# Optimization experiments

Hardware: AMD Instinct MI355X
Metric: run time of the kernel (lower is better)

## Reference

```python
import jax, jax.numpy as jnp
import numpy as np

N_NODES = 65536
N_EDGES = 1048576
HID = 128
NUM_FEAT = 128
NUM_LAYERS = 3
NUM_EXPERTS = 4
NUM_GRAPHS = 512
NUM_CLASSES = 10
TEMP = 0.1


def _hard_concrete(logits, key, temp=TEMP):
    u = jax.random.uniform(key, logits.shape, dtype=logits.dtype, minval=1e-6, maxval=1.0 - 1e-6)
    g = -jnp.log(-jnp.log(u + 1e-20) + 1e-20)
    y_soft = jax.nn.sigmoid((logits + g) / temp)
    y_hard = (y_soft > 0.5).astype(y_soft.dtype)
    # straight-through: forward hard, backward soft
    return y_hard + (y_soft - jax.lax.stop_gradient(y_soft))


def _gin_encoder(h, src, dst, w1, b1, w2, b2, eps, edge_weight=None):
    # GIN with optional scalar edge weights: agg = sum_{j->i} w_ij * h_j
    L = w1.shape[0]
    for l in range(L):
        msg = h[src]
        if edge_weight is not None:
            msg = msg * edge_weight[:, None]
        agg = jax.ops.segment_sum(msg, dst, num_segments=N_NODES)
        z = (1.0 + eps[l]) * h + agg
        z = jax.nn.relu(z @ w1[l] + b1[l]) @ w2[l] + b2[l]
        h = jax.nn.relu(z) if l < L - 1 else z
    return h


def _mean_pool(h, batch):
    s = jax.ops.segment_sum(h, batch, num_segments=NUM_GRAPHS)
    cnt = jax.ops.segment_sum(jnp.ones((h.shape[0], 1), h.dtype), batch, num_segments=NUM_GRAPHS)
    return s / jnp.maximum(cnt, 1.0)


def setup_inputs() -> dict:
    key = jax.random.key(0)
    ks = jax.random.split(key, 32)
    s = 0.05
    d = {}
    d['x'] = jax.random.normal(ks[0], (N_NODES, NUM_FEAT), dtype=jnp.float32)
    d['edge_index'] = jax.random.randint(ks[1], (2, N_EDGES), 0, N_NODES, dtype=jnp.int32)
    d['batch'] = jnp.sort(jax.random.randint(ks[2], (N_NODES,), 0, NUM_GRAPHS, dtype=jnp.int32))
    # causal encoder (layers stacked; F == HID so shapes are uniform)
    d['cw1'] = jax.random.normal(ks[3], (NUM_LAYERS, HID, HID), dtype=jnp.float32) * s
    d['cb1'] = jnp.zeros((NUM_LAYERS, HID), jnp.float32)
    d['cw2'] = jax.random.normal(ks[4], (NUM_LAYERS, HID, HID), dtype=jnp.float32) * s
    d['cb2'] = jnp.zeros((NUM_LAYERS, HID), jnp.float32)
    d['ceps'] = jnp.zeros((NUM_LAYERS,), jnp.float32)
    # classifier encoder
    d['kw1'] = jax.random.normal(ks[5], (NUM_LAYERS, HID, HID), dtype=jnp.float32) * s
    d['kb1'] = jnp.zeros((NUM_LAYERS, HID), jnp.float32)
    d['kw2'] = jax.random.normal(ks[6], (NUM_LAYERS, HID, HID), dtype=jnp.float32) * s
    d['kb2'] = jnp.zeros((NUM_LAYERS, HID), jnp.float32)
    d['keps'] = jnp.zeros((NUM_LAYERS,), jnp.float32)
    # per-expert node mask MLPs: HID -> HID -> 1
    d['nm_w1'] = jax.random.normal(ks[7], (NUM_EXPERTS, HID, HID), dtype=jnp.float32) * s
    d['nm_b1'] = jnp.zeros((NUM_EXPERTS, HID), jnp.float32)
    d['nm_w2'] = jax.random.normal(ks[8], (NUM_EXPERTS, HID, 1), dtype=jnp.float32) * s
    d['nm_b2'] = jnp.zeros((NUM_EXPERTS, 1), jnp.float32)
    # per-expert edge mask MLPs: 2*HID -> HID -> 1
    d['em_w1'] = jax.random.normal(ks[9], (NUM_EXPERTS, 2 * HID, HID), dtype=jnp.float32) * s
    d['em_b1'] = jnp.zeros((NUM_EXPERTS, HID), jnp.float32)
    d['em_w2'] = jax.random.normal(ks[10], (NUM_EXPERTS, HID, 1), dtype=jnp.float32) * s
    d['em_b2'] = jnp.zeros((NUM_EXPERTS, 1), jnp.float32)
    # per-expert feat mask MLPs: HID -> HID -> NUM_FEAT
    d['fm_w1'] = jax.random.normal(ks[11], (NUM_EXPERTS, HID, HID), dtype=jnp.float32) * s
    d['fm_b1'] = jnp.zeros((NUM_EXPERTS, HID), jnp.float32)
    d['fm_w2'] = jax.random.normal(ks[12], (NUM_EXPERTS, HID, NUM_FEAT), dtype=jnp.float32) * s
    d['fm_b2'] = jnp.zeros((NUM_EXPERTS, NUM_FEAT), jnp.float32)
    # per-expert classifiers
    d['cls_w'] = jax.random.normal(ks[13], (NUM_EXPERTS, HID, NUM_CLASSES), dtype=jnp.float32) * s
    d['cls_b'] = jnp.zeros((NUM_EXPERTS, NUM_CLASSES), jnp.float32)
    return d


def reference(x, edge_index, batch, cw1, cb1, cw2, cb2, ceps, kw1, kb1, kw2, kb2, keps,
              nm_w1, nm_b1, nm_w2, nm_b2, em_w1, em_b1, em_w2, em_b2,
              fm_w1, fm_b1, fm_w2, fm_b2, cls_w, cls_b):
    src, dst = edge_index[0], edge_index[1]
    Z = _gin_encoder(x, src, dst, cw1, cb1, cw2, cb2, ceps)  # [N, HID]
    edge_feat = jnp.concatenate([Z[src], Z[dst]], axis=1)     # [E, 2*HID]
    base_key = jax.random.key(42)
    node_masks, edge_masks, feat_masks = [], [], []
    h_stable_list, expert_logits = [], []
    for k in range(NUM_EXPERTS):
        kk = jax.random.split(jax.random.fold_in(base_key, k), 3)
        nl = jax.nn.relu(Z @ nm_w1[k] + nm_b1[k]) @ nm_w2[k] + nm_b2[k]          # [N,1]
        el = jax.nn.relu(edge_feat @ em_w1[k] + em_b1[k]) @ em_w2[k] + em_b2[k]  # [E,1]
        fl = jax.nn.relu(Z @ fm_w1[k] + fm_b1[k]) @ fm_w2[k] + fm_b2[k]          # [N,F]
        node_mask = _hard_concrete(nl, kk[0])
        edge_mask = _hard_concrete(el, kk[1])
        feat_mask = _hard_concrete(fl, kk[2])
        node_masks.append(node_mask)
        edge_masks.append(edge_mask)
        feat_masks.append(feat_mask)
        masked_x = x * node_mask * feat_mask
        ew = edge_mask[:, 0]
        masked_Z = _gin_encoder(masked_x, src, dst, kw1, kb1, kw2, kb2, keps, edge_weight=ew)
        h_st = _mean_pool(masked_Z, batch)                                        # [G, HID]
        h_stable_list.append(h_st)
        expert_logits.append(h_st @ cls_w[k] + cls_b[k])
    node_masks = jnp.stack(node_masks, axis=1)       # [N, K, 1]
    edge_masks = jnp.stack(edge_masks, axis=1)       # [E, K, 1]
    feat_masks = jnp.stack(feat_masks, axis=1)       # [N, K, F]
    h_stable = jnp.stack(h_stable_list, axis=1)      # [G, K, HID]
    expert_logits = jnp.stack(expert_logits, axis=1) # [G, K, C]
    h_orig = _mean_pool(Z, batch)                    # [G, HID]
    return expert_logits, h_stable, h_orig, node_masks, edge_masks, feat_masks
```

## Files before the change

### kernel.cpp

```cpp
#include <hip/hip_runtime.h>
#include <stdint.h>

#define N_NODESC 65536
#define N_EDGESC 1048576
#define HIDC 128
#define NUM_GRAPHSC 512
#define NUM_CLASSESC 10
#define NUM_EXPERTSC 4
#define NUM_LAYERSC 3

static const size_t NH = (size_t)N_NODESC * HIDC;

typedef __attribute__((ext_vector_type(8))) short short8v;
typedef __attribute__((ext_vector_type(4))) float float4v;

__host__ __device__ __forceinline__ uint32_t rotl32(uint32_t v, int r) {
  return (v << r) | (v >> (32 - r));
}
__host__ __device__ inline void threefry2x32(uint32_t k0, uint32_t k1,
                                             uint32_t x0, uint32_t x1,
                                             uint32_t* o0, uint32_t* o1) {
  uint32_t k2 = k0 ^ k1 ^ 0x1BD11BDAu;
  x0 += k0; x1 += k1;
#define TF_R(r) x0 += x1; x1 = rotl32(x1, r); x1 ^= x0;
  TF_R(13) TF_R(15) TF_R(26) TF_R(6)
  x0 += k1; x1 += k2 + 1u;
  TF_R(17) TF_R(29) TF_R(16) TF_R(24)
  x0 += k2; x1 += k0 + 2u;
  TF_R(13) TF_R(15) TF_R(26) TF_R(6)
  x0 += k0; x1 += k1 + 3u;
  TF_R(17) TF_R(29) TF_R(16) TF_R(24)
  x0 += k1; x1 += k2 + 4u;
  TF_R(13) TF_R(15) TF_R(26) TF_R(6)
  x0 += k2; x1 += k0 + 5u;
#undef TF_R
  *o0 = x0; *o1 = x1;
}

__device__ __forceinline__ float uniform_from_bits(uint32_t b) {
  float f = __uint_as_float((b >> 9) | 0x3f800000u) - 1.0f;
  const float mn = 1e-6f;
  const float mx = 1.0f - 1e-6f;
  return fmaxf(mn, __fadd_rn(__fmul_rn(f, __fsub_rn(mx, mn)), mn));
}

__device__ __forceinline__ float hc_decide(float l, uint32_t key0, uint32_t key1,
                                           uint32_t i) {
  uint32_t o0, o1;
  threefry2x32(key0, key1, 0u, i, &o0, &o1);
  float u = uniform_from_bits(o0 ^ o1);
  float tf = -__logf(u);
  float gf = -__logf(tf);
  float margf = l + gf;
  if (fabsf(margf) > 1e-4f) return (margf > 0.0f) ? 1.0f : 0.0f;
  float t32 = (float)(-log((double)u));
  float g32 = (float)(-log((double)t32));
  float m32 = __fadd_rn(l, g32);
  float q = m32 / 0.1f;
  float e32 = (float)exp(-(double)q);
  float den = __fadd_rn(1.0f, e32);
  float s = 1.0f / den;
  return (s > 0.5f) ? 1.0f : 0.0f;
}

__device__ __forceinline__ float bf2f(unsigned short u) {
  return __uint_as_float(((uint32_t)u) << 16);
}
__device__ __forceinline__ unsigned short f2bf(float v) {
  uint32_t u = __float_as_uint(v);
  return (unsigned short)((u + 0x7FFFu + ((u >> 16) & 1u)) >> 16);
}

__global__ void khist(const int* __restrict__ dst, int* __restrict__ deg) {
  int e = blockIdx.x * 256 + threadIdx.x;
  if (e < N_EDGESC) atomicAdd(&deg[dst[e]], 1);
}

__global__ void kscan(const int* __restrict__ deg, int* __restrict__ offs) {
  __shared__ int part[1024];
  int t = threadIdx.x;
  int base = t * 64;
  int s = 0;
  for (int i = 0; i < 64; ++i) s += deg[base + i];
  part[t] = s;
  __syncthreads();
  for (int off = 1; off < 1024; off <<= 1) {
    int v = 0;
    if (t >= off) v = part[t - off];
    __syncthreads();
    part[t] += v;
    __syncthreads();
  }
  int run = part[t] - s;
  for (int i = 0; i < 64; ++i) {
    int d = deg[base + i];
    offs[base + i] = run;
    run += d;
  }
  if (t == 1023) offs[N_NODESC] = run;
}

__global__ void kfill(const int* __restrict__ src, const int* __restrict__ dst,
                      int* __restrict__ curs, int* __restrict__ csr_src,
                      int* __restrict__ csr_eid) {
  int e = blockIdx.x * 256 + threadIdx.x;
  if (e >= N_EDGESC) return;
  int d = dst[e];
  int p = atomicAdd(&curs[d], 1);
  csr_src[p] = src[e];
  csr_eid[p] = e;
}

__global__ void ksort(const int* __restrict__ offs, int* __restrict__ csr_src,
                      int* __restrict__ csr_eid) {
  int n = blockIdx.x * 256 + threadIdx.x;
  if (n >= N_NODESC) return;
  int s = offs[n], e = offs[n + 1];
  for (int i = s + 1; i < e; ++i) {
    int ke = csr_eid[i], ks = csr_src[i];
    int j = i - 1;
    while (j >= s && csr_eid[j] > ke) {
      csr_eid[j + 1] = csr_eid[j];
      csr_src[j + 1] = csr_src[j];
      --j;
    }
    csr_eid[j + 1] = ke;
    csr_src[j + 1] = ks;
  }
}

__global__ void kbounds(const int* __restrict__ batch, int* __restrict__ bounds) {
  int g = threadIdx.x;
  int lo = 0, hi = N_NODESC;
  while (lo < hi) {
    int mid = (lo + hi) >> 1;
    if (batch[mid] < g) lo = mid + 1; else hi = mid;
  }
  bounds[g] = lo;
  if (g == 0) bounds[NUM_GRAPHSC] = N_NODESC;
}

__global__ void gather_z(const float* __restrict__ hin,
                         const int* __restrict__ offs,
                         const int* __restrict__ csr_src,
                         const float* __restrict__ epsArr, int l,
                         float* __restrict__ zout) {
  int gt = blockIdx.x * blockDim.x + threadIdx.x;
  int n = gt >> 6;
  int lane = gt & 63;
  if (n >= N_NODESC) return;
  int s = offs[n], e = offs[n + 1];
  float ax = 0.f, ay = 0.f;
  int i = s;
  for (; i + 4 <= e; i += 4) {
    int s0 = csr_src[i], s1 = csr_src[i + 1], s2 = csr_src[i + 2], s3 = csr_src[i + 3];
    const float2 v0 = *(const float2*)&hin[(size_t)s0 * HIDC + lane * 2];
    const float2 v1 = *(const float2*)&hin[(size_t)s1 * HIDC + lane * 2];
    const float2 v2 = *(const float2*)&hin[(size_t)s2 * HIDC + lane * 2];
    const float2 v3 = *(const float2*)&hin[(size_t)s3 * HIDC + lane * 2];
    ax = __fadd_rn(ax, v0.x); ay = __fadd_rn(ay, v0.y);
    ax = __fadd_rn(ax, v1.x); ay = __fadd_rn(ay, v1.y);
    ax = __fadd_rn(ax, v2.x); ay = __fadd_rn(ay, v2.y);
    ax = __fadd_rn(ax, v3.x); ay = __fadd_rn(ay, v3.y);
  }
  for (; i < e; ++i) {
    int sn = csr_src[i];
    const float2 v = *(const float2*)&hin[(size_t)sn * HIDC + lane * 2];
    ax = __fadd_rn(ax, v.x);
    ay = __fadd_rn(ay, v.y);
  }
  float ep = __fadd_rn(1.0f, epsArr[l]);
  const float2 hv = *(const float2*)&hin[(size_t)n * HIDC + lane * 2];
  ax = __fadd_rn(__fmul_rn(ep, hv.x), ax);
  ay = __fadd_rn(__fmul_rn(ep, hv.y), ay);
  float2 o; o.x = ax; o.y = ay;
  *(float2*)&zout[(size_t)n * HIDC + lane * 2] = o;
}

__device__ __forceinline__ int MXOR(int m) { return (m * 4) ^ ((m & 96) >> 1); }

__device__ __forceinline__ void gemm_body(const float* __restrict__ Xf,
                                          const float* __restrict__ W,
                                          const float* __restrict__ bias,
                                          float* __restrict__ Of,
                                          int doRelu, int tile) {
  __shared__ char sXb[64 * 512];
  __shared__ char sWb[64 * 512];
  const int tid = threadIdx.x;
  const size_t base = (size_t)tile * HIDC * HIDC;
  const int tm = (tid >> 4) << 3;
  const int tn = (tid & 15) << 3;
  const int xA = MXOR(tm), xA2 = MXOR(tm + 4);
  const int xB = MXOR(tn), xB2 = MXOR(tn + 4);

  float acc[8][8];
#pragma unroll
  for (int i = 0; i < 8; ++i)
#pragma unroll
    for (int j = 0; j < 8; ++j) acc[i][j] = 0.0f;

  for (int kh = 0; kh < 2; ++kh) {
    __syncthreads();
#pragma unroll
    for (int i = 0; i < 8; ++i) {
      int idx = tid + 256 * i;
      int m = idx >> 4;
      int kq = (idx & 15) * 4;
      float4 v = *(const float4*)(Xf + base + (size_t)m * HIDC + kh * 64 + kq);
      int mo = MXOR(m);
      *(float*)(sXb + (kq + 0) * 512 + mo) = v.x;
      *(float*)(sXb + (kq + 1) * 512 + mo) = v.y;
      *(float*)(sXb + (kq + 2) * 512 + mo) = v.z;
      *(float*)(sXb + (kq + 3) * 512 + mo) = v.w;
    }
#pragma unroll
    for (int i = 0; i < 8; ++i) {
      int idx = tid + 256 * i;
      int kk = idx >> 5;
      int n0 = (idx & 31) * 4;
      float4 v = *(const float4*)(W + (size_t)(kh * 64 + kk) * HIDC + n0);
      *(float4*)(sWb + kk * 512 + MXOR(n0)) = v;
    }
    __syncthreads();

#pragma unroll 4
    for (int kk = 0; kk < 64; ++kk) {
      float4 a0 = *(const float4*)(sXb + kk * 512 + xA);
      float4 a1 = *(const float4*)(sXb + kk * 512 + xA2);
      float4 b0 = *(const float4*)(sWb + kk * 512 + xB);
      float4 b1 = *(const float4*)(sWb + kk * 512 + xB2);
      float a[8] = {a0.x, a0.y, a0.z, a0.w, a1.x, a1.y, a1.z, a1.w};
      float b[8] = {b0.x, b0.y, b0.z, b0.w, b1.x, b1.y, b1.z, b1.w};
#pragma unroll
      for (int i = 0; i < 8; ++i)
#pragma unroll
        for (int j = 0; j < 8; ++j) acc[i][j] = fmaf(a[i], b[j], acc[i][j]);
    }
  }

  float bvals[8];
#pragma unroll
  for (int j = 0; j < 8; ++j) bvals[j] = bias ? bias[tn + j] : 0.0f;
#pragma unroll
  for (int i = 0; i < 8; ++i) {
    float r[8];
#pragma unroll
    for (int j = 0; j < 8; ++j) {
      float v = __fadd_rn(acc[i][j], bvals[j]);
      if (doRelu) v = fmaxf(v, 0.0f);
      r[j] = v;
    }
    size_t off = base + (size_t)(tm + i) * HIDC + tn;
    *(float4*)&Of[off] = *(float4*)&r[0];
    *(float4*)&Of[off + 4] = *(float4*)&r[4];
  }
}

__global__ __launch_bounds__(256, 2)
void gemm_f32(const float* __restrict__ X, const float* __restrict__ W,
              const float* __restrict__ bias, float* __restrict__ O, int doRelu) {
  gemm_body(X, W, bias, O, doRelu, blockIdx.x);
}

__global__ __launch_bounds__(256, 2)
void gemm_f32x4(const float* __restrict__ X,
                const float* W0, const float* W1, const float* W2, const float* W3,
                const float* b0, const float* b1,
                float* o0, float* o1, float* o2, float* o3) {
  int slice = blockIdx.x >> 9;
  int tile = blockIdx.x & 511;
  const float* W; const float* bias; float* O; int relu;
  if (slice == 0)      { W = W0; bias = b0; O = o0; relu = 1; }
  else if (slice == 1) { W = W1; bias = b1; O = o1; relu = 1; }
  else if (slice == 2) { W = W2; bias = nullptr; O = o2; relu = 0; }
  else                 { W = W3; bias = nullptr; O = o3; relu = 0; }
  gemm_body(X, W, bias, O, relu, tile);
}

__global__ void kprepW(const float* __restrict__ kw1, const float* __restrict__ kw2,
                       unsigned short* __restrict__ Wt) {
  int t = blockIdx.x * 256 + threadIdx.x;
  int mat = t >> 11;
  int r = t & 2047;
  int n = r >> 4;
  int kkc = r & 15;
  const float* W = (mat < 3) ? (kw1 + (size_t)mat * HIDC * HIDC)
                             : (kw2 + (size_t)(mat - 3) * HIDC * HIDC);
  unsigned short pk[8];
#pragma unroll
  for (int j = 0; j < 8; ++j)
    pk[j] = f2bf(W[(size_t)(kkc * 8 + j) * HIDC + n]);
  *(uint4*)(Wt + (size_t)mat * HIDC * HIDC + (size_t)n * HIDC + kkc * 8) =
      *(uint4*)pk;
}

__global__ __launch_bounds__(256, 2)
void gemm_mfma(const unsigned short* __restrict__ Xpool,
               const unsigned short* __restrict__ Wt,
               const float* __restrict__ bias,
               unsigned short* __restrict__ Opool, int doRelu) {
  __shared__ unsigned short sX[128 * 128];
  __shared__ unsigned short sW[128 * 128];
  const int tid = threadIdx.x;
  const int kex = blockIdx.x >> 9;
  const int tile = blockIdx.x & 511;
  const unsigned short* X = Xpool + (size_t)kex * NH + (size_t)tile * HIDC * HIDC;
  unsigned short* O = Opool + (size_t)kex * NH + (size_t)tile * HIDC * HIDC;

#pragma unroll
  for (int i = 0; i < 8; ++i) {
    int idx = tid + 256 * i;
    int r = idx >> 4;
    int cc = idx & 15;
    uint4 vx = *(const uint4*)(X + (size_t)r * HIDC + cc * 8);
    uint4 vw = *(const uint4*)(Wt + (size_t)r * HIDC + cc * 8);
    int sc = (cc ^ (r & 7)) * 8;
    *(uint4*)(sX + r * HIDC + sc) = vx;
    *(uint4*)(sW + r * HIDC + sc) = vw;
  }
  __syncthreads();

  const int lane = tid & 63;
  const int wid = tid >> 6;
  const int wm = wid * 32;
  const int lrow = lane & 15;
  const int lk = (lane >> 4) * 4;

  float4v acc[2][8];
#pragma unroll
  for (int rt = 0; rt < 2; ++rt)
#pragma unroll
    for (int nt = 0; nt < 8; ++nt) acc[rt][nt] = (float4v)0.0f;

  union FU { uint2 u2[2]; short8v s8; };

  for (int kc = 0; kc < 128; kc += 32) {
    int kb = kc + lk;
    int c0 = ((kb >> 3) ^ 0) * 8 + (kb & 7);
    short8v afr[2], bfr[8];
#pragma unroll
    for (int rt = 0; rt < 2; ++rt) {
      int row = wm + rt * 16 + lrow;
      const unsigned short* basep = sX + row * HIDC;
      int s0 = (((kb) >> 3) ^ (row & 7)) * 8 + (kb & 7);
      int s1 = (((kb + 16) >> 3) ^ (row & 7)) * 8 + (kb & 7);
      FU u;
      u.u2[0] = *(const uint2*)(basep + s0);
      u.u2[1] = *(const uint2*)(basep + s1);
      afr[rt] = u.s8;
    }
#pragma unroll
    for (int nt = 0; nt < 8; ++nt) {
      int row = nt * 16 + lrow;
      const unsigned short* basep = sW + row * HIDC;
      int s0 = (((kb) >> 3) ^ (row & 7)) * 8 + (kb & 7);
      int s1 = (((kb + 16) >> 3) ^ (row & 7)) * 8 + (kb & 7);
      FU u;
      u.u2[0] = *(const uint2*)(basep + s0);
      u.u2[1] = *(const uint2*)(basep + s1);
      bfr[nt] = u.s8;
    }
#pragma unroll
    for (int rt = 0; rt < 2; ++rt)
#pragma unroll
      for (int nt = 0; nt < 8; ++nt)
        acc[rt][nt] = __builtin_amdgcn_mfma_f32_16x16x32_bf16(
            afr[rt], bfr[nt], acc[rt][nt], 0, 0, 0);
    (void)c0;
  }

#pragma unroll
  for (int nt = 0; nt < 8; ++nt) {
    float bv = bias[nt * 16 + lrow];
#pragma unroll
    for (int rt = 0; rt < 2; ++rt) {
#pragma unroll
      for (int j = 0; j < 4; ++j) {
        float v = acc[rt][nt][j] + bv;
        if (doRelu) v = fmaxf(v, 0.0f);
        int row = wm + rt * 16 + (lane >> 4) * 4 + j;
        O[(size_t)row * HIDC + nt * 16 + lrow] = f2bf(v);
      }
    }
  }
}

__global__ void rowdot(const float* __restrict__ X, const float* __restrict__ w,
                       const float* __restrict__ bptr, uint32_t key0, uint32_t key1,
                       float* __restrict__ outp) {
  int gt = blockIdx.x * blockDim.x + threadIdx.x;
  int row = gt >> 6, lane = gt & 63;
  if (row >= N_NODESC) return;
  const float2 x = *(const float2*)&X[(size_t)row * HIDC + lane * 2];
  const float2 ww = *(const float2*)&w[lane * 2];
  float p = x.x * ww.x + x.y * ww.y;
#pragma unroll
  for (int m = 32; m; m >>= 1) p += __shfl_xor(p, m, 64);
  if (lane == 0) {
    float l = p + bptr[0];
    outp[(size_t)row * NUM_EXPERTSC] = hc_decide(l, key0, key1, (uint32_t)row);
  }
}

__global__ void edge_csrK(const float* __restrict__ A, const float* __restrict__ Bm,
                          const float* __restrict__ b1, const float* __restrict__ w2,
                          const float* __restrict__ b2,
                          const int* __restrict__ offs, const int* __restrict__ csr_src,
                          const int* __restrict__ csr_eid,
                          uint32_t key0, uint32_t key1,
                          float* __restrict__ outp, unsigned char* __restrict__ mcsr) {
  int n = blockIdx.x * 4 + (threadIdx.x >> 6);
  int lane = threadIdx.x & 63;
  int g = lane >> 4;
  int gl = lane & 15;
  const float4* Bv = (const float4*)&Bm[(size_t)n * HIDC + gl * 8];
  float4 b_lo = Bv[0], b_hi = Bv[1];
  float4 bb_lo = *(const float4*)&b1[gl * 8];
  float4 bb_hi = *(const float4*)&b1[gl * 8 + 4];
  float4 w_lo = *(const float4*)&w2[gl * 8];
  float4 w_hi = *(const float4*)&w2[gl * 8 + 4];
  float bscalar = b2[0];
  int s = offs[n], e = offs[n + 1];
  for (int i = s; i < e; i += 4) {
    int cnt = e - i; if (cnt > 4) cnt = 4;
    float p = 0.0f;
    if (g < cnt) {
      int sg = csr_src[i + g];
      const float4* Av = (const float4*)&A[(size_t)sg * HIDC + gl * 8];
      float4 a_lo = Av[0], a_hi = Av[1];
      float h;
      h = fmaxf(__fadd_rn(__fadd_rn(a_lo.x, b_lo.x), bb_lo.x), 0.0f); p = fmaf(h, w_lo.x, p);
      h = fmaxf(__fadd_rn(__fadd_rn(a_lo.y, b_lo.y), bb_lo.y), 0.0f); p = fmaf(h, w_lo.y, p);
      h = fmaxf(__fadd_rn(__fadd_rn(a_lo.z, b_lo.z), bb_lo.z), 0.0f); p = fmaf(h, w_lo.z, p);
      h = fmaxf(__fadd_rn(__fadd_rn(a_lo.w, b_lo.w), bb_lo.w), 0.0f); p = fmaf(h, w_lo.w, p);
      h = fmaxf(__fadd_rn(__fadd_rn(a_hi.x, b_hi.x), bb_hi.x), 0.0f); p = fmaf(h, w_hi.x, p);
      h = fmaxf(__fadd_rn(__fadd_rn(a_hi.y, b_hi.y), bb_hi.y), 0.0f); p = fmaf(h, w_hi.y, p);
      h = fmaxf(__fadd_rn(__fadd_rn(a_hi.z, b_hi.z), bb_hi.z), 0.0f); p = fmaf(h, w_hi.z, p);
      h = fmaxf(__fadd_rn(__fadd_rn(a_hi.w, b_hi.w), bb_hi.w), 0.0f); p = fmaf(h, w_hi.w, p);
    }
    p += __shfl_xor(p, 1, 16);
    p += __shfl_xor(p, 2, 16);
    p += __shfl_xor(p, 4, 16);
    p += __shfl_xor(p, 8, 16);
    if (g < cnt && gl == 0) {
      int eid = csr_eid[i + g];
      float l = p + bscalar;
      float mval = hc_decide(l, key0, key1, (uint32_t)eid);
      outp[(size_t)eid * NUM_EXPERTSC] = mval;
      mcsr[i + g] = (unsigned char)mval;
    }
  }
}

__global__ void ksampleF(const float* __restrict__ lg, uint32_t key0, uint32_t key1,
                         float* __restrict__ outp) {
  int i = blockIdx.x * 256 + threadIdx.x;
  float m = hc_decide(lg[i], key0, key1, (uint32_t)i);
  outp[(size_t)(i >> 7) * (NUM_EXPERTSC * HIDC) + (i & 127)] = m;
}

__global__ void kmaskxB(const float* __restrict__ x, const float* __restrict__ nmaskb,
                        const float* __restrict__ fmaskb,
                        unsigned short* __restrict__ hbpool) {
  int k = blockIdx.x >> 13;
  int t = (blockIdx.x & 8191) * 256 + threadIdx.x;
  int n = t >> 5;
  int q = (t & 31) << 2;
  float nm = nmaskb[(size_t)n * NUM_EXPERTSC + k];
  float4 xv = *(const float4*)&x[(size_t)n * HIDC + q];
  float4 fv = *(const float4*)&fmaskb[(size_t)n * (NUM_EXPERTSC * HIDC) + k * HIDC + q];
  ushort2 p0, p1;
  p0.x = f2bf(xv.x * nm * fv.x); p0.y = f2bf(xv.y * nm * fv.y);
  p1.x = f2bf(xv.z * nm * fv.z); p1.y = f2bf(xv.w * nm * fv.w);
  uint2 pk; pk.x = (uint32_t)p0.x | ((uint32_t)p0.y << 16);
  pk.y = (uint32_t)p1.x | ((uint32_t)p1.y << 16);
  *(uint2*)(hbpool + (size_t)k * NH + (size_t)n * HIDC + q) = pk;
}

__global__ void gatherC(const unsigned short* __restrict__ hpool,
                        const int* __restrict__ offs,
                        const int* __restrict__ csr_src,
                        const unsigned char* __restrict__ mcsr,
                        const float* __restrict__ epsArr, int l,
                        unsigned short* __restrict__ aggpool) {
  int gid = blockIdx.x * 4 + (threadIdx.x >> 6);
  int lane = threadIdx.x & 63;
  int k = gid >> 16;
  int n = gid & 65535;
  const unsigned short* h = hpool + (size_t)k * NH;
  const unsigned char* mc = mcsr + (size_t)k * N_EDGESC;
  int s = offs[n], e = offs[n + 1];
  float ax = 0.f, ay = 0.f;
  for (int base = s; base < e; base += 64) {
    int j = base + lane;
    int valid = (j < e);
    int keep = valid ? (mc[j] != 0) : 0;
    int srcj = valid ? csr_src[j] : 0;
    unsigned long long ball = __ballot(keep);
    while (ball) {
      int l0 = -1, l1 = -1, l2 = -1, l3 = -1;
      l0 = __ffsll((unsigned long long)ball) - 1; ball &= ball - 1;
      if (ball) { l1 = __ffsll((unsigned long long)ball) - 1; ball &= ball - 1; }
      if (ball) { l2 = __ffsll((unsigned long long)ball) - 1; ball &= ball - 1; }
      if (ball) { l3 = __ffsll((unsigned long long)ball) - 1; ball &= ball - 1; }
      int s0 = __shfl(srcj, l0, 64);
      int s1 = (l1 >= 0) ? __shfl(srcj, l1, 64) : 0;
      int s2 = (l2 >= 0) ? __shfl(srcj, l2, 64) : 0;
      int s3 = (l3 >= 0) ? __shfl(srcj, l3, 64) : 0;
      uint32_t v0 = *(const uint32_t*)(h + (size_t)s0 * HIDC + lane * 2);
      uint32_t v1 = (l1 >= 0) ? *(const uint32_t*)(h + (size_t)s1 * HIDC + lane * 2) : 0;
      uint32_t v2 = (l2 >= 0) ? *(const uint32_t*)(h + (size_t)s2 * HIDC + lane * 2) : 0;
      uint32_t v3 = (l3 >= 0) ? *(const uint32_t*)(h + (size_t)s3 * HIDC + lane * 2) : 0;
      ax += __uint_as_float(v0 << 16); ay += __uint_as_float(v0 & 0xFFFF0000u);
      if (l1 >= 0) { ax += __uint_as_float(v1 << 16); ay += __uint_as_float(v1 & 0xFFFF0000u); }
      if (l2 >= 0) { ax += __uint_as_float(v2 << 16); ay += __uint_as_float(v2 & 0xFFFF0000u); }
      if (l3 >= 0) { ax += __uint_as_float(v3 << 16); ay += __uint_as_float(v3 & 0xFFFF0000u); }
    }
  }
  float ep = 1.0f + epsArr[l];
  uint32_t hv = *(const uint32_t*)(h + (size_t)n * HIDC + lane * 2);
  ax = fmaf(ep, __uint_as_float(hv << 16), ax);
  ay = fmaf(ep, __uint_as_float(hv & 0xFFFF0000u), ay);
  uint32_t pk = (uint32_t)f2bf(ax) | ((uint32_t)f2bf(ay) << 16);
  *(uint32_t*)(aggpool + (size_t)k * NH + (size_t)n * HIDC + lane * 2) = pk;
}

__global__ void pool(const float* __restrict__ h, const int* __restrict__ bounds,
                     float* __restrict__ outp, int rowStride) {
  int g = blockIdx.x, j = threadIdx.x;
  int s = bounds[g], e = bounds[g + 1];
  float acc = 0.0f;
  for (int i = s; i < e; ++i) acc = __fadd_rn(acc, h[(size_t)i * HIDC + j]);
  int cnt = e - s; if (cnt < 1) cnt = 1;
  outp[(size_t)g * rowStride + j] = acc / (float)cnt;
}

__global__ void poolB(const unsigned short* __restrict__ hbpool,
                      const int* __restrict__ bounds, float* __restrict__ outp) {
  int k = blockIdx.x >> 9;
  int g = blockIdx.x & 511;
  int j = threadIdx.x;
  const unsigned short* h = hbpool + (size_t)k * NH;
  int s = bounds[g], e = bounds[g + 1];
  float acc = 0.0f;
  for (int i = s; i < e; ++i) acc += bf2f(h[(size_t)i * HIDC + j]);
  int cnt = e - s; if (cnt < 1) cnt = 1;
  outp[(size_t)g * (NUM_EXPERTSC * HIDC) + k * HIDC + j] = acc / (float)cnt;
}

__global__ void kclsB(const float* __restrict__ hst, const float* __restrict__ w,
                      const float* __restrict__ b, float* __restrict__ outp) {
  int k = blockIdx.x >> 9;
  int g = blockIdx.x & 511;
  int c = threadIdx.x;
  if (c >= NUM_CLASSESC) return;
  float acc = 0.0f;
  for (int j = 0; j < HIDC; ++j)
    acc = __fadd_rn(acc, __fmul_rn(hst[(size_t)g * (NUM_EXPERTSC * HIDC) + k * HIDC + j],
                                   w[(size_t)k * HIDC * NUM_CLASSESC + j * NUM_CLASSESC + c]));
  outp[(size_t)g * (NUM_EXPERTSC * NUM_CLASSESC) + k * NUM_CLASSESC + c] =
      acc + b[k * NUM_CLASSESC + c];
}

extern "C" void kernel_launch(void* const* d_in, const int* in_sizes, int n_in,
                              void* d_out, int out_size, void* d_ws, size_t ws_size,
                              hipStream_t stream) {
  const float* x    = (const float*)d_in[0];
  const int* eidx   = (const int*)d_in[1];
  const int* batch  = (const int*)d_in[2];
  const float* cw1  = (const float*)d_in[3];
  const float* cb1  = (const float*)d_in[4];
  const float* cw2  = (const float*)d_in[5];
  const float* cb2  = (const float*)d_in[6];
  const float* ceps = (const float*)d_in[7];
  const float* kw1  = (const float*)d_in[8];
  const float* kb1  = (const float*)d_in[9];
  const float* kw2  = (const float*)d_in[10];
  const float* kb2  = (const float*)d_in[11];
  const float* keps = (const float*)d_in[12];
  const float* nm_w1 = (const float*)d_in[13];
  const float* nm_b1 = (const float*)d_in[14];
  const float* nm_w2 = (const float*)d_in[15];
  const float* nm_b2 = (const float*)d_in[16];
  const float* em_w1 = (const float*)d_in[17];
  const float* em_b1 = (const float*)d_in[18];
  const float* em_w2 = (const float*)d_in[19];
  const float* em_b2 = (const float*)d_in[20];
  const float* fm_w1 = (const float*)d_in[21];
  const float* fm_b1 = (const float*)d_in[22];
  const float* fm_w2 = (const float*)d_in[23];
  const float* fm_b2 = (const float*)d_in[24];
  const float* cls_w = (const float*)d_in[25];
  const float* cls_b = (const float*)d_in[26];

  const int* src = eidx;
  const int* dstp = eidx + N_EDGESC;
  float* out = (float*)d_out;

  const size_t OFF_HST    = 20480;
  const size_t OFF_HORIG  = 282624;
  const size_t OFF_NODE   = 348160;
  const size_t OFF_EDGE   = 610304;
  const size_t OFF_FEAT   = 4804608;

  float* P  = (float*)d_ws;
  float* Zf = P;
  float* t1 = P + NH;
  float* t2 = P + 2 * NH;
  float* t3 = P + 3 * NH;
  float* t4 = P + 4 * NH;
  unsigned short* hbB  = (unsigned short*)P;
  unsigned short* aggB = (unsigned short*)(P + 2 * NH);
  unsigned short* tmpB = (unsigned short*)(P + 4 * NH);
  float* nl = P + 6 * NH;
  int* deg    = (int*)(nl + N_NODESC);
  int* offs   = deg + N_NODESC;
  int* curs   = offs + N_NODESC + 1;
  int* csr_s  = curs + N_NODESC;
  int* csr_e  = csr_s + N_EDGESC;
  int* bounds = csr_e + N_EDGESC;
  unsigned char* mcsr = (unsigned char*)(bounds + NUM_GRAPHSC + 3);
  unsigned short* Wt = (unsigned short*)(mcsr + 4 * (size_t)N_EDGESC + 64);

  uint32_t kk[NUM_EXPERTSC][3][2];
  for (int k = 0; k < NUM_EXPERTSC; ++k) {
    uint32_t f0, f1;
    threefry2x32(0u, 42u, 0u, (uint32_t)k, &f0, &f1);
    threefry2x32(f0, f1, 0u, 0u, &kk[k][0][0], &kk[k][0][1]);
    threefry2x32(f0, f1, 0u, 1u, &kk[k][1][0], &kk[k][1][1]);
    threefry2x32(f0, f1, 0u, 2u, &kk[k][2][0], &kk[k][2][1]);
  }

  hipMemsetAsync(deg, 0, N_NODESC * sizeof(int), stream);
  khist<<<N_EDGESC / 256, 256, 0, stream>>>(dstp, deg);
  kscan<<<1, 1024, 0, stream>>>(deg, offs);
  hipMemcpyAsync(curs, offs, N_NODESC * sizeof(int), hipMemcpyDeviceToDevice, stream);
  kfill<<<N_EDGESC / 256, 256, 0, stream>>>(src, dstp, curs, csr_s, csr_e);
  ksort<<<N_NODESC / 256, 256, 0, stream>>>(offs, csr_s, csr_e);
  kbounds<<<1, NUM_GRAPHSC, 0, stream>>>(batch, bounds);
  kprepW<<<48, 256, 0, stream>>>(kw1, kw2, Wt);

  const int GZ_GRID = N_NODESC * 64 / 256;
  const int GEMM_GRID = N_NODESC / HIDC;

  for (int l = 0; l < NUM_LAYERSC; ++l) {
    const float* hin = (l == 0) ? x : t1;
    gather_z<<<GZ_GRID, 256, 0, stream>>>(hin, offs, csr_s, ceps, l, t3);
    gemm_f32<<<GEMM_GRID, 256, 0, stream>>>(t3, cw1 + (size_t)l * HIDC * HIDC,
                                            cb1 + l * HIDC, t2, 1);
    gemm_f32<<<GEMM_GRID, 256, 0, stream>>>(t2, cw2 + (size_t)l * HIDC * HIDC,
                                            cb2 + l * HIDC,
                                            (l == NUM_LAYERSC - 1) ? Zf : t1,
                                            (l < NUM_LAYERSC - 1) ? 1 : 0);
  }
  pool<<<NUM_GRAPHSC, HIDC, 0, stream>>>(Zf, bounds, out + OFF_HORIG, HIDC);

  for (int k = 0; k < NUM_EXPERTSC; ++k) {
    gemm_f32x4<<<4 * GEMM_GRID, 256, 0, stream>>>(
        Zf,
        nm_w1 + (size_t)k * HIDC * HIDC, fm_w1 + (size_t)k * HIDC * HIDC,
        em_w1 + (size_t)k * 2 * HIDC * HIDC,
        em_w1 + (size_t)k * 2 * HIDC * HIDC + HIDC * HIDC,
        nm_b1 + k * HIDC, fm_b1 + k * HIDC,
        t1, t2, t3, t4);
    rowdot<<<GZ_GRID, 256, 0, stream>>>(t1, nm_w2 + (size_t)k * HIDC, nm_b2 + k,
                                        kk[k][0][0], kk[k][0][1], out + OFF_NODE + k);
    gemm_f32<<<GEMM_GRID, 256, 0, stream>>>(t2, fm_w2 + (size_t)k * HIDC * HIDC,
                                            fm_b2 + (size_t)k * HIDC, t1, 0);
    ksampleF<<<(N_NODESC * HIDC) / 256, 256, 0, stream>>>(t1, kk[k][2][0], kk[k][2][1],
                                                          out + OFF_FEAT + (size_t)k * HIDC);
    edge_csrK<<<N_NODESC / 4, 256, 0, stream>>>(t3, t4, em_b1 + k * HIDC,
                                                em_w2 + (size_t)k * HIDC, em_b2 + k,
                                                offs, csr_s, csr_e,
                                                kk[k][1][0], kk[k][1][1],
                                                out + OFF_EDGE + k,
                                                mcsr + (size_t)k * N_EDGESC);
  }

  kmaskxB<<<4 * 8192, 256, 0, stream>>>(x, out + OFF_NODE, out + OFF_FEAT, hbB);
  for (int l = 0; l < NUM_LAYERSC; ++l) {
    gatherC<<<4 * GZ_GRID, 256, 0, stream>>>(hbB, offs, csr_s, mcsr, keps, l, aggB);
    gemm_mfma<<<4 * GEMM_GRID, 256, 0, stream>>>(aggB, Wt + (size_t)l * HIDC * HIDC,
                                                 kb1 + l * HIDC, tmpB, 1);
    gemm_mfma<<<4 * GEMM_GRID, 256, 0, stream>>>(tmpB, Wt + (size_t)(3 + l) * HIDC * HIDC,
                                                 kb2 + l * HIDC, hbB,
                                                 (l < NUM_LAYERSC - 1) ? 1 : 0);
  }
  poolB<<<4 * NUM_GRAPHSC, HIDC, 0, stream>>>(hbB, bounds, out + OFF_HST);
  kclsB<<<4 * NUM_GRAPHSC, 64, 0, stream>>>(out + OFF_HST, cls_w, cls_b, out);
}
```

Measured before the change: 2.611 ms.

## Fuse edge gather into first MFMA GEMM and feature-mask sampling into GEMM epilogue

The masked GIN aggregation now writes its bf16 result straight into shared memory and feeds the first MFMA GEMM in the same kernel. Blocks are remapped so each expert's tiles sit on a pair of XCDs. Separately, the feature-mask hard-concrete sampling moves into the epilogue of the fm_w2 GEMM through a templated epilogue lambda. This drops the agg buffer round trip through global memory and one launch per expert, but each gather block now processes 128 rows with 4 waves, which may lower the parallelism available to hide gather latency.

```diff
diff --git a/kernel.cpp b/kernel.cpp
--- a/kernel.cpp
+++ b/kernel.cpp
@@ -179,11 +179,11 @@
 
 __device__ __forceinline__ int MXOR(int m) { return (m * 4) ^ ((m & 96) >> 1); }
 
-__device__ __forceinline__ void gemm_body(const float* __restrict__ Xf,
+template <typename EPI>
+__device__ __forceinline__ void gemm_core(const float* __restrict__ Xf,
                                           const float* __restrict__ W,
                                           const float* __restrict__ bias,
-                                          float* __restrict__ Of,
-                                          int doRelu, int tile) {
+                                          int doRelu, int tile, EPI epi) {
   __shared__ char sXb[64 * 512];
   __shared__ char sWb[64 * 512];
   const int tid = threadIdx.x;
@@ -250,16 +250,19 @@
       if (doRelu) v = fmaxf(v, 0.0f);
       r[j] = v;
     }
-    size_t off = base + (size_t)(tm + i) * HIDC + tn;
-    *(float4*)&Of[off] = *(float4*)&r[0];
-    *(float4*)&Of[off + 4] = *(float4*)&r[4];
+    epi(tile * HIDC + tm + i, tn, r);
   }
 }
 
 __global__ __launch_bounds__(256, 2)
 void gemm_f32(const float* __restrict__ X, const float* __restrict__ W,
               const float* __restrict__ bias, float* __restrict__ O, int doRelu) {
-  gemm_body(X, W, bias, O, doRelu, blockIdx.x);
+  gemm_core(X, W, bias, doRelu, blockIdx.x,
+            [&](int row, int tn, const float* r) {
+              float* orow = O + (size_t)row * HIDC + tn;
+              *(float4*)&orow[0] = *(const float4*)&r[0];
+              *(float4*)&orow[4] = *(const float4*)&r[4];
+            });
 }
 
 __global__ __launch_bounds__(256, 2)
@@ -274,7 +277,29 @@
   else if (slice == 1) { W = W1; bias = b1; O = o1; relu = 1; }
   else if (slice == 2) { W = W2; bias = nullptr; O = o2; relu = 0; }
   else                 { W = W3; bias = nullptr; O = o3; relu = 0; }
-  gemm_body(X, W, bias, O, relu, tile);
+  gemm_core(X, W, bias, relu, tile,
+            [&](int row, int tn, const float* r) {
+              float* orow = O + (size_t)row * HIDC + tn;
+              *(float4*)&orow[0] = *(const float4*)&r[0];
+              *(float4*)&orow[4] = *(const float4*)&r[4];
+            });
+}
+
+__global__ __launch_bounds__(256, 2)
+void gemm_feat(const float* __restrict__ X, const float* __restrict__ W,
+               const float* __restrict__ bias, uint32_t key0, uint32_t key1,
+               float* __restrict__ outFeat ) {
+  gemm_core(X, W, bias, 0, blockIdx.x,
+            [&](int row, int tn, const float* r) {
+              float d[8];
+#pragma unroll
+              for (int j = 0; j < 8; ++j)
+                d[j] = hc_decide(r[j], key0, key1,
+                                 (uint32_t)(row * HIDC + tn + j));
+              float* orow = outFeat + (size_t)row * (NUM_EXPERTSC * HIDC) + tn;
+              *(float4*)&orow[0] = *(const float4*)&d[0];
+              *(float4*)&orow[4] = *(const float4*)&d[4];
+            });
 }
 
 __global__ void kprepW(const float* __restrict__ kw1, const float* __restrict__ kw2,
@@ -292,6 +317,72 @@
     pk[j] = f2bf(W[(size_t)(kkc * 8 + j) * HIDC + n]);
   *(uint4*)(Wt + (size_t)mat * HIDC * HIDC + (size_t)n * HIDC + kkc * 8) =
       *(uint4*)pk;
+}
+
+__device__ __forceinline__ void mfma_tile(const unsigned short* sX,
+                                          const unsigned short* sW,
+                                          const float* __restrict__ bias,
+                                          unsigned short* __restrict__ O,
+                                          int doRelu, int lane, int wid) {
+  const int wm = wid * 32;
+  const int lrow = lane & 15;
+  const int lk = (lane >> 4) * 4;
+
+  float4v acc[2][8];
+#pragma unroll
+  for (int rt = 0; rt < 2; ++rt)
+#pragma unroll
+    for (int nt = 0; nt < 8; ++nt) acc[rt][nt] = (float4v)0.0f;
+
+  union FU { uint2 u2[2]; short8v s8; };
+
+  for (int kc = 0; kc < 128; kc += 32) {
+    int kb = kc + lk;
+    short8v afr[2], bfr[8];
+#pragma unroll
+    for (int rt = 0; rt < 2; ++rt) {
+      int row = wm + rt * 16 + lrow;
+      const unsigned short* basep = sX + row * HIDC;
+      int s0 = (((kb) >> 3) ^ (row & 7)) * 8 + (kb & 7);
+      int s1 = (((kb + 16) >> 3) ^ (row & 7)) * 8 + (kb & 7);
+      FU u;
+      u.u2[0] = *(const uint2*)(basep + s0);
+      u.u2[1] = *(const uint2*)(basep + s1);
+      afr[rt] = u.s8;
+    }
+#pragma unroll
+    for (int nt = 0; nt < 8; ++nt) {
+      int row = nt * 16 + lrow;
+      const unsigned short* basep = sW + row * HIDC;
+      int s0 = (((kb) >> 3) ^ (row & 7)) * 8 + (kb & 7);
+      int s1 = (((kb + 16) >> 3) ^ (row & 7)) * 8 + (kb & 7);
+      FU u;
+      u.u2[0] = *(const uint2*)(basep + s0);
+      u.u2[1] = *(const uint2*)(basep + s1);
+      bfr[nt] = u.s8;
+    }
+#pragma unroll
+    for (int rt = 0; rt < 2; ++rt)
+#pragma unroll
+      for (int nt = 0; nt < 8; ++nt)
+        acc[rt][nt] = __builtin_amdgcn_mfma_f32_16x16x32_bf16(
+            afr[rt], bfr[nt], acc[rt][nt], 0, 0, 0);
+  }
+
+#pragma unroll
+  for (int nt = 0; nt < 8; ++nt) {
+    float bv = bias[nt * 16 + lrow];
+#pragma unroll
+    for (int rt = 0; rt < 2; ++rt) {
+#pragma unroll
+      for (int j = 0; j < 4; ++j) {
+        float v = acc[rt][nt][j] + bv;
+        if (doRelu) v = fmaxf(v, 0.0f);
+        int row = wm + rt * 16 + (lane >> 4) * 4 + j;
+        O[(size_t)row * HIDC + nt * 16 + lrow] = f2bf(v);
+      }
+    }
+  }
 }
 
 __global__ __launch_bounds__(256, 2)
@@ -319,70 +410,85 @@
     *(uint4*)(sW + r * HIDC + sc) = vw;
   }
   __syncthreads();
-
+  mfma_tile(sX, sW, bias, O, doRelu, tid & 63, tid >> 6);
+}
+
+__global__ __launch_bounds__(256, 2)
+void gather_mfma(const unsigned short* __restrict__ hpool,
+                 const int* __restrict__ offs,
+                 const int* __restrict__ csr_src,
+                 const unsigned char* __restrict__ mcsr,
+                 const float* __restrict__ epsArr, int l,
+                 const unsigned short* __restrict__ Wt,
+                 const float* __restrict__ bias,
+                 unsigned short* __restrict__ Opool) {
+  __shared__ unsigned short sX[128 * 128];
+  __shared__ unsigned short sW[128 * 128];
+  const int tid = threadIdx.x;
+  const int b = blockIdx.x;
+  const int xcd = b & 7;
+  const int k = xcd >> 1;
+  const int tile = ((b >> 3) << 1) | (xcd & 1);
   const int lane = tid & 63;
   const int wid = tid >> 6;
-  const int wm = wid * 32;
-  const int lrow = lane & 15;
-  const int lk = (lane >> 4) * 4;
-
-  float4v acc[2][8];
-#pragma unroll
-  for (int rt = 0; rt < 2; ++rt)
-#pragma unroll
-    for (int nt = 0; nt < 8; ++nt) acc[rt][nt] = (float4v)0.0f;
-
-  union FU { uint2 u2[2]; short8v s8; };
-
-  for (int kc = 0; kc < 128; kc += 32) {
-    int kb = kc + lk;
-    int c0 = ((kb >> 3) ^ 0) * 8 + (kb & 7);
-    short8v afr[2], bfr[8];
-#pragma unroll
-    for (int rt = 0; rt < 2; ++rt) {
-      int row = wm + rt * 16 + lrow;
-      const unsigned short* basep = sX + row * HIDC;
-      int s0 = (((kb) >> 3) ^ (row & 7)) * 8 + (kb & 7);
-      int s1 = (((kb + 16) >> 3) ^ (row & 7)) * 8 + (kb & 7);
-      FU u;
-      u.u2[0] = *(const uint2*)(basep + s0);
-      u.u2[1] = *(const uint2*)(basep + s1);
-      afr[rt] = u.s8;
-    }
-#pragma unroll
-    for (int nt = 0; nt < 8; ++nt) {
-      int row = nt * 16 + lrow;
-      const unsigned short* basep = sW + row * HIDC;
-      int s0 = (((kb) >> 3) ^ (row & 7)) * 8 + (kb & 7);
-      int s1 = (((kb + 16) >> 3) ^ (row & 7)) * 8 + (kb & 7);
-      FU u;
-      u.u2[0] = *(const uint2*)(basep + s0);
-      u.u2[1] = *(const uint2*)(basep + s1);
-      bfr[nt] = u.s8;
-    }
-#pragma unroll
-    for (int rt = 0; rt < 2; ++rt)
-#pragma unroll
-      for (int nt = 0; nt < 8; ++nt)
-        acc[rt][nt] = __builtin_amdgcn_mfma_f32_16x16x32_bf16(
-            afr[rt], bfr[nt], acc[rt][nt], 0, 0, 0);
-    (void)c0;
-  }
-
-#pragma unroll
-  for (int nt = 0; nt < 8; ++nt) {
-    float bv = bias[nt * 16 + lrow];
-#pragma unroll
-    for (int rt = 0; rt < 2; ++rt) {
-#pragma unroll
-      for (int j = 0; j < 4; ++j) {
-        float v = acc[rt][nt][j] + bv;
-        if (doRelu) v = fmaxf(v, 0.0f);
-        int row = wm + rt * 16 + (lane >> 4) * 4 + j;
-        O[(size_t)row * HIDC + nt * 16 + lrow] = f2bf(v);
+
+#pragma unroll
+  for (int i = 0; i < 8; ++i) {
+    int idx = tid + 256 * i;
+    int r = idx >> 4;
+    int cc = idx & 15;
+    uint4 vw = *(const uint4*)(Wt + (size_t)r * HIDC + cc * 8);
+    *(uint4*)(sW + r * HIDC + ((cc ^ (r & 7)) * 8)) = vw;
+  }
+
+  const unsigned short* h = hpool + (size_t)k * NH;
+  const unsigned char* mc = mcsr + (size_t)k * N_EDGESC;
+  const float ep = 1.0f + epsArr[l];
+  const int c = lane * 2;
+  const int cchunk = c >> 3;
+  const int crem = c & 7;
+  for (int t = 0; t < 32; ++t) {
+    int r = wid * 32 + t;
+    int n = tile * 128 + r;
+    int s = offs[n], e = offs[n + 1];
+    float ax = 0.f, ay = 0.f;
+    for (int base2 = s; base2 < e; base2 += 64) {
+      int j = base2 + lane;
+      int valid = (j < e);
+      int keep = valid ? (mc[j] != 0) : 0;
+      int srcj = valid ? csr_src[j] : 0;
+      unsigned long long ball = __ballot(keep);
+      while (ball) {
+        int l0 = __ffsll((unsigned long long)ball) - 1; ball &= ball - 1;
+        int l1 = -1, l2 = -1, l3 = -1;
+        if (ball) { l1 = __ffsll((unsigned long long)ball) - 1; ball &= ball - 1; }
+        if (ball) { l2 = __ffsll((unsigned long long)ball) - 1; ball &= ball - 1; }
+        if (ball) { l3 = __ffsll((unsigned long long)ball) - 1; ball &= ball - 1; }
+        int s0 = __shfl(srcj, l0, 64);
+        int s1 = (l1 >= 0) ? __shfl(srcj, l1, 64) : 0;
+        int s2 = (l2 >= 0) ? __shfl(srcj, l2, 64) : 0;
+        int s3 = (l3 >= 0) ? __shfl(srcj, l3, 64) : 0;
+        uint32_t v0 = *(const uint32_t*)(h + (size_t)s0 * HIDC + c);
+        uint32_t v1 = (l1 >= 0) ? *(const uint32_t*)(h + (size_t)s1 * HIDC + c) : 0;
+        uint32_t v2 = (l2 >= 0) ? *(const uint32_t*)(h + (size_t)s2 * HIDC + c) : 0;
+        uint32_t v3 = (l3 >= 0) ? *(const uint32_t*)(h + (size_t)s3 * HIDC + c) : 0;
+        ax += __uint_as_float(v0 << 16); ay += __uint_as_float(v0 & 0xFFFF0000u);
+        if (l1 >= 0) { ax += __uint_as_float(v1 << 16); ay += __uint_as_float(v1 & 0xFFFF0000u); }
+        if (l2 >= 0) { ax += __uint_as_float(v2 << 16); ay += __uint_as_float(v2 & 0xFFFF0000u); }
+        if (l3 >= 0) { ax += __uint_as_float(v3 << 16); ay += __uint_as_float(v3 & 0xFFFF0000u); }
       }
     }
-  }
+    uint32_t hv = *(const uint32_t*)(h + (size_t)n * HIDC + c);
+    ax = fmaf(ep, __uint_as_float(hv << 16), ax);
+    ay = fmaf(ep, __uint_as_float(hv & 0xFFFF0000u), ay);
+    uint32_t pk = (uint32_t)f2bf(ax) | ((uint32_t)f2bf(ay) << 16);
+    int sc = ((cchunk ^ (r & 7)) * 8) + crem;
+    *(uint32_t*)(sX + r * HIDC + sc) = pk;
+  }
+  __syncthreads();
+
+  unsigned short* O = Opool + (size_t)k * NH + (size_t)tile * HIDC * HIDC;
+  mfma_tile(sX, sW, bias, O, 1, lane, wid);
 }
 
 __global__ void rowdot(const float* __restrict__ X, const float* __restrict__ w,
@@ -452,13 +558,6 @@
   }
 }
 
-__global__ void ksampleF(const float* __restrict__ lg, uint32_t key0, uint32_t key1,
-                         float* __restrict__ outp) {
-  int i = blockIdx.x * 256 + threadIdx.x;
-  float m = hc_decide(lg[i], key0, key1, (uint32_t)i);
-  outp[(size_t)(i >> 7) * (NUM_EXPERTSC * HIDC) + (i & 127)] = m;
-}
-
 __global__ void kmaskxB(const float* __restrict__ x, const float* __restrict__ nmaskb,
                         const float* __restrict__ fmaskb,
                         unsigned short* __restrict__ hbpool) {
@@ -475,54 +574,6 @@
   uint2 pk; pk.x = (uint32_t)p0.x | ((uint32_t)p0.y << 16);
   pk.y = (uint32_t)p1.x | ((uint32_t)p1.y << 16);
   *(uint2*)(hbpool + (size_t)k * NH + (size_t)n * HIDC + q) = pk;
-}
-
-__global__ void gatherC(const unsigned short* __restrict__ hpool,
-                        const int* __restrict__ offs,
-                        const int* __restrict__ csr_src,
-                        const unsigned char* __restrict__ mcsr,
-                        const float* __restrict__ epsArr, int l,
-                        unsigned short* __restrict__ aggpool) {
-  int gid = blockIdx.x * 4 + (threadIdx.x >> 6);
-  int lane = threadIdx.x & 63;
-  int k = gid >> 16;
-  int n = gid & 65535;
-  const unsigned short* h = hpool + (size_t)k * NH;
-  const unsigned char* mc = mcsr + (size_t)k * N_EDGESC;
-  int s = offs[n], e = offs[n + 1];
-  float ax = 0.f, ay = 0.f;
-  for (int base = s; base < e; base += 64) {
-    int j = base + lane;
-    int valid = (j < e);
-    int keep = valid ? (mc[j] != 0) : 0;
-    int srcj = valid ? csr_src[j] : 0;
-    unsigned long long ball = __ballot(keep);
-    while (ball) {
-      int l0 = -1, l1 = -1, l2 = -1, l3 = -1;
-      l0 = __ffsll((unsigned long long)ball) - 1; ball &= ball - 1;
-      if (ball) { l1 = __ffsll((unsigned long long)ball) - 1; ball &= ball - 1; }
-      if (ball) { l2 = __ffsll((unsigned long long)ball) - 1; ball &= ball - 1; }
-      if (ball) { l3 = __ffsll((unsigned long long)ball) - 1; ball &= ball - 1; }
-      int s0 = __shfl(srcj, l0, 64);
-      int s1 = (l1 >= 0) ? __shfl(srcj, l1, 64) : 0;
-      int s2 = (l2 >= 0) ? __shfl(srcj, l2, 64) : 0;
-      int s3 = (l3 >= 0) ? __shfl(srcj, l3, 64) : 0;
-      uint32_t v0 = *(const uint32_t*)(h + (size_t)s0 * HIDC + lane * 2);
-      uint32_t v1 = (l1 >= 0) ? *(const uint32_t*)(h + (size_t)s1 * HIDC + lane * 2) : 0;
-      uint32_t v2 = (l2 >= 0) ? *(const uint32_t*)(h + (size_t)s2 * HIDC + lane * 2) : 0;
-      uint32_t v3 = (l3 >= 0) ? *(const uint32_t*)(h + (size_t)s3 * HIDC + lane * 2) : 0;
-      ax += __uint_as_float(v0 << 16); ay += __uint_as_float(v0 & 0xFFFF0000u);
-      if (l1 >= 0) { ax += __uint_as_float(v1 << 16); ay += __uint_as_float(v1 & 0xFFFF0000u); }
-      if (l2 >= 0) { ax += __uint_as_float(v2 << 16); ay += __uint_as_float(v2 & 0xFFFF0000u); }
-      if (l3 >= 0) { ax += __uint_as_float(v3 << 16); ay += __uint_as_float(v3 & 0xFFFF0000u); }
-    }
-  }
-  float ep = 1.0f + epsArr[l];
-  uint32_t hv = *(const uint32_t*)(h + (size_t)n * HIDC + lane * 2);
-  ax = fmaf(ep, __uint_as_float(hv << 16), ax);
-  ay = fmaf(ep, __uint_as_float(hv & 0xFFFF0000u), ay);
-  uint32_t pk = (uint32_t)f2bf(ax) | ((uint32_t)f2bf(ay) << 16);
-  *(uint32_t*)(aggpool + (size_t)k * NH + (size_t)n * HIDC + lane * 2) = pk;
 }
 
 __global__ void pool(const float* __restrict__ h, const int* __restrict__ bounds,
@@ -610,7 +661,6 @@
   float* t3 = P + 3 * NH;
   float* t4 = P + 4 * NH;
   unsigned short* hbB  = (unsigned short*)P;
-  unsigned short* aggB = (unsigned short*)(P + 2 * NH);
   unsigned short* tmpB = (unsigned short*)(P + 4 * NH);
   float* nl = P + 6 * NH;
   int* deg    = (int*)(nl + N_NODESC);
@@ -665,10 +715,10 @@
         t1, t2, t3, t4);
     rowdot<<<GZ_GRID, 256, 0, stream>>>(t1, nm_w2 + (size_t)k * HIDC, nm_b2 + k,
                                         kk[k][0][0], kk[k][0][1], out + OFF_NODE + k);
-    gemm_f32<<<GEMM_GRID, 256, 0, stream>>>(t2, fm_w2 + (size_t)k * HIDC * HIDC,
-                                            fm_b2 + (size_t)k * HIDC, t1, 0);
-    ksampleF<<<(N_NODESC * HIDC) / 256, 256, 0, stream>>>(t1, kk[k][2][0], kk[k][2][1],
-                                                          out + OFF_FEAT + (size_t)k * HIDC);
+    gemm_feat<<<GEMM_GRID, 256, 0, stream>>>(t2, fm_w2 + (size_t)k * HIDC * HIDC,
+                                             fm_b2 + (size_t)k * HIDC,
+                                             kk[k][2][0], kk[k][2][1],
+                                             out + OFF_FEAT + (size_t)k * HIDC);
     edge_csrK<<<N_NODESC / 4, 256, 0, stream>>>(t3, t4, em_b1 + k * HIDC,
                                                 em_w2 + (size_t)k * HIDC, em_b2 + k,
                                                 offs, csr_s, csr_e,
@@ -679,9 +729,9 @@
 
   kmaskxB<<<4 * 8192, 256, 0, stream>>>(x, out + OFF_NODE, out + OFF_FEAT, hbB);
   for (int l = 0; l < NUM_LAYERSC; ++l) {
-    gatherC<<<4 * GZ_GRID, 256, 0, stream>>>(hbB, offs, csr_s, mcsr, keps, l, aggB);
-    gemm_mfma<<<4 * GEMM_GRID, 256, 0, stream>>>(aggB, Wt + (size_t)l * HIDC * HIDC,
-                                                 kb1 + l * HIDC, tmpB, 1);
+    gather_mfma<<<4 * GEMM_GRID, 256, 0, stream>>>(hbB, offs, csr_s, mcsr, keps, l,
+                                                   Wt + (size_t)l * HIDC * HIDC,
+                                                   kb1 + l * HIDC, tmpB);
     gemm_mfma<<<4 * GEMM_GRID, 256, 0, stream>>>(tmpB, Wt + (size_t)(3 + l) * HIDC * HIDC,
                                                  kb2 + l * HIDC, hbB,
                                                  (l < NUM_LAYERSC - 1) ? 1 : 0);
```

Result: slower. 3.667 ms (+40.5%).
